# Kernel optimization log

Measured on AMD Instinct MI355X. Metric: run time of the kernel, lower is better.

The kernel has to match this reference:

```python
import jax, jax.numpy as jnp
import numpy as np

N_NODES = 100000
N_EDGES = 1600000
X_DIM, E_DIM = 4, 39


def setup_inputs() -> dict:
    key = jax.random.key(0)
    ks = jax.random.split(key, 12)
    x = jax.random.normal(ks[0], (N_NODES, X_DIM), dtype=jnp.float32)
    edge_index = jax.random.randint(ks[1], (2, N_EDGES), 0, N_NODES, dtype=jnp.int64)
    edge_attr = jax.random.normal(ks[2], (N_EDGES, E_DIM), dtype=jnp.float32)
    def lin(k, fan_in, fan_out):
        kw, kb = jax.random.split(k)
        bound = 1.0 / np.sqrt(fan_in)
        W = jax.random.uniform(kw, (fan_in, fan_out), jnp.float32, -bound, bound)
        b = jax.random.uniform(kb, (fan_out,), jnp.float32, -bound, bound)
        return W, b
    W1, b1 = lin(ks[3], 43, 64)
    W2, b2 = lin(ks[4], 64, 128)
    W3, b3 = lin(ks[5], 132, 256)
    W4, b4 = lin(ks[6], 256, 256)
    return {"x": x, "edge_index": edge_index, "edge_attr": edge_attr,
            "W1": W1, "b1": b1, "W2": W2, "b2": b2,
            "W3": W3, "b3": b3, "W4": W4, "b4": b4}


def reference(x, edge_index, edge_attr, W1, b1, W2, b2, W3, b3, W4, b4):
    row, col = edge_index[0], edge_index[1]
    n = x.shape[0]
    # gather source-node features, concat edge attrs -> edge MLP
    h = jnp.concatenate([x[col], edge_attr], axis=1)            # [E, 43]
    h = jax.nn.relu(h @ W1 + b1)                                # [E, 64]
    h = jax.nn.relu(h @ W2 + b2)                                # [E, 128]
    # scatter_mean over edges grouped by destination node `row`
    s = jax.ops.segment_sum(h, row, num_segments=n)             # [N, 128]
    cnt = jax.ops.segment_sum(jnp.ones((row.shape[0],), h.dtype), row,
                              num_segments=n)                   # [N]
    mean = s / jnp.maximum(cnt, 1.0)[:, None]                   # 0 for empty segments
    # concat node features with aggregated messages -> node MLP
    o = jnp.concatenate([x, mean], axis=1)                      # [N, 132]
    o = jax.nn.relu(o @ W3 + b3)                                # [N, 256]
    o = jax.nn.relu(o @ W4 + b4)                                # [N, 256]
    return o
```

## Files before the change

kernel.cpp:

```cpp
#include <hip/hip_runtime.h>
#include <hip/hip_bf16.h>

#define NN 100000
#define NE 1600000
#define XD 4
#define ED 39
#define K1 43
#define H1 64
#define H2 128
#define H3 256
#define NBN 16
#define NBK2 32
#define NCHUNK 98

typedef short bfrag8 __attribute__((ext_vector_type(8)));
typedef float facc4  __attribute__((ext_vector_type(4)));
typedef unsigned short u16x4 __attribute__((ext_vector_type(4)));

static __device__ __forceinline__ unsigned short f2bf(float f) {
    __hip_bfloat16 b = __float2bfloat16(f);
    union { __hip_bfloat16 b; unsigned short u; } v; v.b = b;
    return v.u;
}
static __device__ __forceinline__ float bf2f(unsigned short h) {
    union { unsigned int u; float f; } v; v.u = ((unsigned int)h) << 16;
    return v.f;
}

__global__ __launch_bounds__(256) void hist_kernel(const int* __restrict__ eidx,
                                                   int* __restrict__ cnt) {
    int e = blockIdx.x * 256 + threadIdx.x;
    if (e < NE) atomicAdd(&cnt[eidx[e]], 1);
}

__global__ __launch_bounds__(1024) void scan1_kernel(const int* __restrict__ cnt,
                                                     int* __restrict__ row_ptr,
                                                     int* __restrict__ cursor,
                                                     int* __restrict__ chunkSum) {
    __shared__ int wsum[16];
    const int t = threadIdx.x, lane = t & 63, w = t >> 6;
    const int i = blockIdx.x * 1024 + t;
    int v = (i < NN) ? cnt[i] : 0;
    int s = v;
    #pragma unroll
    for (int d = 1; d < 64; d <<= 1) {
        int u = __shfl_up(s, d, 64);
        if (lane >= d) s += u;
    }
    if (lane == 63) wsum[w] = s;
    __syncthreads();
    if (w == 0 && lane < 16) {
        int e = wsum[lane];
        #pragma unroll
        for (int d = 1; d < 16; d <<= 1) {
            int u = __shfl_up(e, d, 64);
            if (lane >= d) e += u;
        }
        wsum[lane] = e;
    }
    __syncthreads();
    int woff = (w == 0) ? 0 : wsum[w - 1];
    if (i < NN) {
        int incl = woff + s;
        row_ptr[i + 1] = incl;
        cursor[i]      = incl - v;
    }
    if (t == 0) chunkSum[blockIdx.x] = wsum[15];
}

__global__ __launch_bounds__(64) void scan2_kernel(const int* __restrict__ chunkSum,
                                                   int* __restrict__ chunkOff) {
    const int lane = threadIdx.x;
    int a = (lane < NCHUNK) ? chunkSum[lane] : 0;
    int b = (lane + 64 < NCHUNK) ? chunkSum[lane + 64] : 0;
    int sa = a;
    #pragma unroll
    for (int d = 1; d < 64; d <<= 1) {
        int u = __shfl_up(sa, d, 64);
        if (lane >= d) sa += u;
    }
    int totA = __shfl(sa, 63, 64);
    int sb = b;
    #pragma unroll
    for (int d = 1; d < 64; d <<= 1) {
        int u = __shfl_up(sb, d, 64);
        if (lane >= d) sb += u;
    }
    sb += totA;
    if (lane < NCHUNK) chunkOff[lane] = sa - a;
    if (lane + 64 < NCHUNK) chunkOff[lane + 64] = sb - b;
}

__global__ __launch_bounds__(1024) void scan3_kernel(const int* __restrict__ chunkOff,
                                                     int* __restrict__ row_ptr,
                                                     int* __restrict__ cursor) {
    const int i = blockIdx.x * 1024 + threadIdx.x;
    const int off = chunkOff[blockIdx.x];
    if (i < NN) {
        row_ptr[i + 1] += off;
        cursor[i]      += off;
    }
    if (i == 0) row_ptr[0] = 0;
}

__global__ __launch_bounds__(256) void build_kernel(const int* __restrict__ eidx,
                                                    int* __restrict__ cursor,
                                                    int* __restrict__ perm) {
    int e = blockIdx.x * 256 + threadIdx.x;
    if (e < NE) {
        int r = eidx[e];
        int pos = atomicAdd(&cursor[r], 1);
        perm[pos] = e;
    }
}

__global__ __launch_bounds__(256) void prep_kernel(
    const float* __restrict__ W1, const float* __restrict__ W2,
    const float* __restrict__ W3, const float* __restrict__ W4,
    unsigned short* __restrict__ W1h, unsigned short* __restrict__ W1l,
    unsigned short* __restrict__ W2h, unsigned short* __restrict__ W2l,
    unsigned short* __restrict__ W3h, unsigned short* __restrict__ W3l,
    unsigned short* __restrict__ W4h, unsigned short* __restrict__ W4l)
{
    int i = blockIdx.x * 256 + threadIdx.x;
    if (i >= 4096 + 8192 + 40960 + 65536) return;
    unsigned short *ph, *pl;
    int idx, col, k;
    float w;
    if (i < 4096) {
        idx = i;
        int grp = idx >> 9, lane = (idx >> 3) & 63, j = idx & 7;
        int wid = grp >> 1, ks = grp & 1;
        col = wid * 16 + (lane & 15);
        k   = ks * 32 + (lane >> 4) * 8 + j;
        w = (k < K1) ? W1[k * H1 + col] : 0.f;
        ph = W1h; pl = W1l;
    } else if (i < 12288) {
        idx = i - 4096;
        int grp = idx >> 9, lane = (idx >> 3) & 63, j = idx & 7;
        int wid = grp >> 2, nt = (grp >> 1) & 1, ks = grp & 1;
        col = wid * 32 + nt * 16 + (lane & 15);
        k   = ks * 32 + (lane >> 4) * 8 + j;
        w = W2[k * H2 + col];
        ph = W2h; pl = W2l;
    } else if (i < 53248) {
        idx = i - 12288;
        int grp = idx >> 9, lane = (idx >> 3) & 63, j = idx & 7;
        int w_ = grp / 20, rem = grp - w_ * 20;
        int ks = rem >> 2, nt = rem & 3;
        col = w_ * 64 + nt * 16 + (lane & 15);
        k   = ks * 32 + (lane >> 4) * 8 + j;
        w = (k < 132) ? W3[k * H3 + col] : 0.f;
        ph = W3h; pl = W3l;
    } else {
        idx = i - 53248;
        int grp = idx >> 9, lane = (idx >> 3) & 63, j = idx & 7;
        int w_ = grp >> 5, rem = grp & 31;
        int ks = rem >> 2, nt = rem & 3;
        col = w_ * 64 + nt * 16 + (lane & 15);
        k   = ks * 32 + (lane >> 4) * 8 + j;
        w = W4[k * H3 + col];
        ph = W4h; pl = W4l;
    }
    unsigned short h = f2bf(w);
    ph[idx] = h;
    pl[idx] = f2bf(w - bf2f(h));
}

__global__ __launch_bounds__(256, 3) void edge_agg_kernel(
    const float* __restrict__ x, const int* __restrict__ eidx,
    const float* __restrict__ ea,
    const unsigned short* __restrict__ W1h, const unsigned short* __restrict__ W1l,
    const float* __restrict__ b1,
    const unsigned short* __restrict__ W2h, const unsigned short* __restrict__ W2l,
    const float* __restrict__ b2,
    const int* __restrict__ row_ptr, const int* __restrict__ perm,
    float* __restrict__ mean)
{
    __shared__ __align__(16) unsigned short uMem[4 * 64 * 72];
    __shared__ __align__(16) int sNode[72];
    __shared__ int sPerm[2][64], sCol[2][64], sRP[NBN + 1];

    unsigned short* Ahi   = uMem;
    unsigned short* Alo   = uMem + 64 * 72;
    unsigned short* H1hi  = uMem + 2 * 64 * 72;
    unsigned short* H1lo  = uMem + 3 * 64 * 72;
    unsigned short* H2Thi = uMem;
    unsigned short* H2Tlo = uMem + 128 * 72;

    const int t    = threadIdx.x;
    const int lane = t & 63;
    const int wid  = t >> 6;
    const int cl   = lane & 15;
    const int lg   = lane >> 4;
    const int n0   = blockIdx.x * NBN;

    int p0 = -1, c0 = 0;
    if (t < 64) {
        int b0  = row_ptr[n0];
        int e0r = row_ptr[n0 + NBN];
        if (b0 + t < e0r) p0 = perm[b0 + t];
        if (p0 >= 0) c0 = eidx[NE + p0];
    }

    if (t <= NBN) sRP[t] = row_ptr[n0 + t];

    bfrag8 w1h_[2], w1l_[2], w2h_[2][2], w2l_[2][2];
    #pragma unroll
    for (int ks = 0; ks < 2; ks++) {
        const int off = ((wid * 2 + ks) * 64 + lane) * 8;
        w1h_[ks] = *(const bfrag8*)&W1h[off];
        w1l_[ks] = *(const bfrag8*)&W1l[off];
    }
    #pragma unroll
    for (int nt = 0; nt < 2; nt++)
        #pragma unroll
        for (int ks = 0; ks < 2; ks++) {
            const int off = (((wid * 2 + nt) * 2 + ks) * 64 + lane) * 8;
            w2h_[nt][ks] = *(const bfrag8*)&W2h[off];
            w2l_[nt][ks] = *(const bfrag8*)&W2l[off];
        }
    const float bias1 = b1[wid * 16 + cl];
    const float bias2[2] = { b2[wid * 32 + cl], b2[wid * 32 + 16 + cl] };

    facc4 acc_sel[2];
    #pragma unroll
    for (int nt = 0; nt < 2; nt++) {
        acc_sel[nt][0] = 0.f; acc_sel[nt][1] = 0.f;
        acc_sel[nt][2] = 0.f; acc_sel[nt][3] = 0.f;
    }

    if (t < 64) { sPerm[0][t] = p0; sCol[0][t] = c0; }
    __syncthreads();

    const int base = sRP[0], cntE = sRP[NBN] - base;

    auto loadA = [&](float (&pv)[4][4], const int* sP, const int* sC) {
        #pragma unroll
        for (int r = 0; r < 4; r++) {
            const int e  = (t >> 4) + r * 16;
            const int k0 = (t & 15) * 4;
            const int ee = sP[e];
            if (ee >= 0) {
                if (k0 == 0) {
                    float4 xv = *(const float4*)&x[(size_t)sC[e] * XD];
                    pv[r][0] = xv.x; pv[r][1] = xv.y; pv[r][2] = xv.z; pv[r][3] = xv.w;
                } else {
                    const float* er = ea + (size_t)ee * ED;
                    #pragma unroll
                    for (int q = 0; q < 4; q++) {
                        int k = k0 + q;
                        pv[r][q] = (k < K1) ? er[k - XD] : 0.f;
                    }
                }
            } else {
                pv[r][0] = pv[r][1] = pv[r][2] = pv[r][3] = 0.f;
            }
        }
    };

    if (cntE > 0) {
        float pv[4][4];
        loadA(pv, sPerm[0], sCol[0]);
        int buf = 0;

        for (int tb = 0; tb < cntE; tb += 64) {
            const int nv   = min(64, cntE - tb);
            const int nbuf = buf ^ 1;

            int pp = -1;
            if (t < 64 && tb + 64 < cntE)
                pp = (tb + 64 + t < cntE) ? perm[base + tb + 64 + t] : -1;

            #pragma unroll
            for (int r = 0; r < 4; r++) {
                const int e  = (t >> 4) + r * 16;
                const int k0 = (t & 15) * 4;
                u16x4 hv, lv;
                #pragma unroll
                for (int q = 0; q < 4; q++) {
                    unsigned short h = f2bf(pv[r][q]);
                    hv[q] = h;
                    lv[q] = f2bf(pv[r][q] - bf2f(h));
                }
                *(u16x4*)&Ahi[e * 72 + k0] = hv;
                *(u16x4*)&Alo[e * 72 + k0] = lv;
            }
            if (t < 72) {
                int nd = -1;
                if (t < nv) {
                    int idx = tb + t;
                    nd = 0;
                    #pragma unroll
                    for (int k = 1; k < 16; k++) nd += ((sRP[k] - base) <= idx);
                }
                sNode[t] = nd;
            }
            __syncthreads();

            int pc = 0;
            if (t < 64 && pp >= 0) pc = eidx[NE + pp];

            facc4 acc1[4];
            #pragma unroll
            for (int mt = 0; mt < 4; mt++) {
                acc1[mt][0] = bias1; acc1[mt][1] = bias1;
                acc1[mt][2] = bias1; acc1[mt][3] = bias1;
            }
            #pragma unroll
            for (int ks = 0; ks < 2; ks++) {
                #pragma unroll
                for (int mt = 0; mt < 4; mt++) {
                    const int ao = (mt * 16 + cl) * 72 + ks * 32 + lg * 8;
                    bfrag8 ah = *(const bfrag8*)&Ahi[ao];
                    bfrag8 al = *(const bfrag8*)&Alo[ao];
                    acc1[mt] = __builtin_amdgcn_mfma_f32_16x16x32_bf16(ah, w1h_[ks], acc1[mt], 0, 0, 0);
                    acc1[mt] = __builtin_amdgcn_mfma_f32_16x16x32_bf16(al, w1h_[ks], acc1[mt], 0, 0, 0);
                    acc1[mt] = __builtin_amdgcn_mfma_f32_16x16x32_bf16(ah, w1l_[ks], acc1[mt], 0, 0, 0);
                }
            }
            #pragma unroll
            for (int mt = 0; mt < 4; mt++)
                #pragma unroll
                for (int j = 0; j < 4; j++) {
                    float v = fmaxf(acc1[mt][j], 0.f);
                    unsigned short h = f2bf(v);
                    int m = mt * 16 + lg * 4 + j;
                    H1hi[m * 72 + wid * 16 + cl] = h;
                    H1lo[m * 72 + wid * 16 + cl] = f2bf(v - bf2f(h));
                }
            if (t < 64) { sPerm[nbuf][t] = pp; sCol[nbuf][t] = pc; }
            __syncthreads();

            if (tb + 64 < cntE) loadA(pv, sPerm[nbuf], sCol[nbuf]);

            facc4 acc2[4][2];
            #pragma unroll
            for (int mt = 0; mt < 4; mt++)
                #pragma unroll
                for (int nt = 0; nt < 2; nt++) {
                    acc2[mt][nt][0] = bias2[nt]; acc2[mt][nt][1] = bias2[nt];
                    acc2[mt][nt][2] = bias2[nt]; acc2[mt][nt][3] = bias2[nt];
                }
            #pragma unroll
            for (int ks = 0; ks < 2; ks++) {
                #pragma unroll
                for (int mt = 0; mt < 4; mt++) {
                    const int ao = (mt * 16 + cl) * 72 + ks * 32 + lg * 8;
                    bfrag8 ah = *(const bfrag8*)&H1hi[ao];
                    bfrag8 al = *(const bfrag8*)&H1lo[ao];
                    #pragma unroll
                    for (int nt = 0; nt < 2; nt++) {
                        acc2[mt][nt] = __builtin_amdgcn_mfma_f32_16x16x32_bf16(ah, w2h_[nt][ks], acc2[mt][nt], 0, 0, 0);
                        acc2[mt][nt] = __builtin_amdgcn_mfma_f32_16x16x32_bf16(al, w2h_[nt][ks], acc2[mt][nt], 0, 0, 0);
                        acc2[mt][nt] = __builtin_amdgcn_mfma_f32_16x16x32_bf16(ah, w2l_[nt][ks], acc2[mt][nt], 0, 0, 0);
                    }
                }
            }
            __syncthreads();

            #pragma unroll
            for (int mt = 0; mt < 4; mt++)
                #pragma unroll
                for (int nt = 0; nt < 2; nt++) {
                    const int c2 = wid * 32 + nt * 16 + cl;
                    u16x4 hv, lv;
                    #pragma unroll
                    for (int j = 0; j < 4; j++) {
                        float v = fmaxf(acc2[mt][nt][j], 0.f);
                        unsigned short h = f2bf(v);
                        hv[j] = h;
                        lv[j] = f2bf(v - bf2f(h));
                    }
                    const int eb = mt * 16 + lg * 4;
                    *(u16x4*)&H2Thi[c2 * 72 + eb] = hv;
                    *(u16x4*)&H2Tlo[c2 * 72 + eb] = lv;
                }
            __syncthreads();

            #pragma unroll
            for (int ks = 0; ks < 2; ks++) {
                const int4* np = (const int4*)&sNode[ks * 32 + lg * 8];
                int4 na = np[0], nb = np[1];
                bfrag8 sf;
                sf[0] = (na.x == cl) ? (short)0x3F80 : (short)0;
                sf[1] = (na.y == cl) ? (short)0x3F80 : (short)0;
                sf[2] = (na.z == cl) ? (short)0x3F80 : (short)0;
                sf[3] = (na.w == cl) ? (short)0x3F80 : (short)0;
                sf[4] = (nb.x == cl) ? (short)0x3F80 : (short)0;
                sf[5] = (nb.y == cl) ? (short)0x3F80 : (short)0;
                sf[6] = (nb.z == cl) ? (short)0x3F80 : (short)0;
                sf[7] = (nb.w == cl) ? (short)0x3F80 : (short)0;
                #pragma unroll
                for (int nt = 0; nt < 2; nt++) {
                    const int hb = (wid * 32 + nt * 16 + cl) * 72 + ks * 32 + lg * 8;
                    bfrag8 hh = *(const bfrag8*)&H2Thi[hb];
                    bfrag8 hl = *(const bfrag8*)&H2Tlo[hb];
                    acc_sel[nt] = __builtin_amdgcn_mfma_f32_16x16x32_bf16(sf, hh, acc_sel[nt], 0, 0, 0);
                    acc_sel[nt] = __builtin_amdgcn_mfma_f32_16x16x32_bf16(sf, hl, acc_sel[nt], 0, 0, 0);
                }
            }
            __syncthreads();
            buf = nbuf;
        }
    }

    #pragma unroll
    for (int nt = 0; nt < 2; nt++)
        #pragma unroll
        for (int j = 0; j < 4; j++) {
            const int n = lg * 4 + j;
            const int deg = sRP[n + 1] - sRP[n];
            const float inv = (deg > 0) ? 1.f / (float)deg : 0.f;
            mean[(size_t)(n0 + n) * H2 + wid * 32 + nt * 16 + cl] = acc_sel[nt][j] * inv;
        }
}

__global__ __launch_bounds__(256, 3) void node_kernel(
    const float* __restrict__ x,
    const float* __restrict__ mean,
    const unsigned short* __restrict__ W3h, const unsigned short* __restrict__ W3l,
    const float* __restrict__ b3,
    const unsigned short* __restrict__ W4h, const unsigned short* __restrict__ W4l,
    const float* __restrict__ b4,
    float* __restrict__ out)
{
    __shared__ __align__(16) unsigned short uM[2 * 32 * 264];
    unsigned short* Ah = uM;
    unsigned short* Al = uM + 32 * 168;
    unsigned short* Hh = uM;
    unsigned short* Hl = uM + 32 * 264;

    const int t    = threadIdx.x;
    const int lane = t & 63;
    const int w    = t >> 6;
    const int cl   = lane & 15;
    const int lg   = lane >> 4;
    const int n0   = blockIdx.x * NBK2;

    {
        const int n   = t & 31;
        const int kq0 = t >> 5;
        #pragma unroll
        for (int it = 0; it < 5; it++) {
            const int k0 = (kq0 + it * 8) * 4;
            float v[4];
            if (k0 == 0) {
                float4 xv = *(const float4*)&x[(size_t)(n0 + n) * XD];
                v[0] = xv.x; v[1] = xv.y; v[2] = xv.z; v[3] = xv.w;
            } else if (k0 <= 128) {
                float4 mv = *(const float4*)&mean[(size_t)(n0 + n) * H2 + (k0 - XD)];
                v[0] = mv.x; v[1] = mv.y; v[2] = mv.z; v[3] = mv.w;
            } else {
                v[0] = v[1] = v[2] = v[3] = 0.f;
            }
            u16x4 hv, lv;
            #pragma unroll
            for (int q = 0; q < 4; q++) {
                unsigned short h = f2bf(v[q]);
                hv[q] = h;
                lv[q] = f2bf(v[q] - bf2f(h));
            }
            *(u16x4*)&Ah[n * 168 + k0] = hv;
            *(u16x4*)&Al[n * 168 + k0] = lv;
        }
    }
    __syncthreads();

    facc4 acc[2][4];
    #pragma unroll
    for (int nt = 0; nt < 4; nt++) {
        float b = b3[w * 64 + nt * 16 + cl];
        #pragma unroll
        for (int mt = 0; mt < 2; mt++) {
            acc[mt][nt][0] = b; acc[mt][nt][1] = b;
            acc[mt][nt][2] = b; acc[mt][nt][3] = b;
        }
    }
    #pragma unroll
    for (int ks = 0; ks < 5; ks++) {
        bfrag8 ah[2], al[2];
        #pragma unroll
        for (int mt = 0; mt < 2; mt++) {
            const int ao = (mt * 16 + cl) * 168 + ks * 32 + lg * 8;
            ah[mt] = *(const bfrag8*)&Ah[ao];
            al[mt] = *(const bfrag8*)&Al[ao];
        }
        #pragma unroll
        for (int nt = 0; nt < 4; nt++) {
            const int wo = (((w * 5 + ks) * 4 + nt) * 64 + lane) * 8;
            bfrag8 bh = *(const bfrag8*)&W3h[wo];
            bfrag8 bl = *(const bfrag8*)&W3l[wo];
            #pragma unroll
            for (int mt = 0; mt < 2; mt++) {
                acc[mt][nt] = __builtin_amdgcn_mfma_f32_16x16x32_bf16(ah[mt], bh, acc[mt][nt], 0, 0, 0);
                acc[mt][nt] = __builtin_amdgcn_mfma_f32_16x16x32_bf16(al[mt], bh, acc[mt][nt], 0, 0, 0);
                acc[mt][nt] = __builtin_amdgcn_mfma_f32_16x16x32_bf16(ah[mt], bl, acc[mt][nt], 0, 0, 0);
            }
        }
    }
    __syncthreads();

    #pragma unroll
    for (int mt = 0; mt < 2; mt++)
        #pragma unroll
        for (int nt = 0; nt < 4; nt++)
            #pragma unroll
            for (int j = 0; j < 4; j++) {
                float v = fmaxf(acc[mt][nt][j], 0.f);
                const int r = mt * 16 + lg * 4 + j;
                const int c = w * 64 + nt * 16 + cl;
                unsigned short h = f2bf(v);
                Hh[r * 264 + c] = h;
                Hl[r * 264 + c] = f2bf(v - bf2f(h));
            }
    __syncthreads();

    facc4 acc2[2][4];
    #pragma unroll
    for (int nt = 0; nt < 4; nt++) {
        float b = b4[w * 64 + nt * 16 + cl];
        #pragma unroll
        for (int mt = 0; mt < 2; mt++) {
            acc2[mt][nt][0] = b; acc2[mt][nt][1] = b;
            acc2[mt][nt][2] = b; acc2[mt][nt][3] = b;
        }
    }
    #pragma unroll
    for (int ks = 0; ks < 8; ks++) {
        bfrag8 ah[2], al[2];
        #pragma unroll
        for (int mt = 0; mt < 2; mt++) {
            const int ao = (mt * 16 + cl) * 264 + ks * 32 + lg * 8;
            ah[mt] = *(const bfrag8*)&Hh[ao];
            al[mt] = *(const bfrag8*)&Hl[ao];
        }
        #pragma unroll
        for (int nt = 0; nt < 4; nt++) {
            const int wo = (((w * 8 + ks) * 4 + nt) * 64 + lane) * 8;
            bfrag8 bh = *(const bfrag8*)&W4h[wo];
            bfrag8 bl = *(const bfrag8*)&W4l[wo];
            #pragma unroll
            for (int mt = 0; mt < 2; mt++) {
                acc2[mt][nt] = __builtin_amdgcn_mfma_f32_16x16x32_bf16(ah[mt], bh, acc2[mt][nt], 0, 0, 0);
                acc2[mt][nt] = __builtin_amdgcn_mfma_f32_16x16x32_bf16(al[mt], bh, acc2[mt][nt], 0, 0, 0);
                acc2[mt][nt] = __builtin_amdgcn_mfma_f32_16x16x32_bf16(ah[mt], bl, acc2[mt][nt], 0, 0, 0);
            }
        }
    }
    #pragma unroll
    for (int mt = 0; mt < 2; mt++)
        #pragma unroll
        for (int nt = 0; nt < 4; nt++)
            #pragma unroll
            for (int j = 0; j < 4; j++)
                out[(size_t)(n0 + mt * 16 + lg * 4 + j) * H3 + w * 64 + nt * 16 + cl] =
                    fmaxf(acc2[mt][nt][j], 0.f);
}

extern "C" void kernel_launch(void* const* d_in, const int* in_sizes, int n_in,
                              void* d_out, int out_size, void* d_ws, size_t ws_size,
                              hipStream_t stream) {
    const float* x    = (const float*)d_in[0];
    const int*   eidx = (const int*)  d_in[1];
    const float* ea   = (const float*)d_in[2];
    const float* W1   = (const float*)d_in[3];
    const float* b1   = (const float*)d_in[4];
    const float* W2   = (const float*)d_in[5];
    const float* b2   = (const float*)d_in[6];
    const float* W3   = (const float*)d_in[7];
    const float* b3   = (const float*)d_in[8];
    const float* W4   = (const float*)d_in[9];
    const float* b4   = (const float*)d_in[10];
    float* out = (float*)d_out;

    char* p = (char*)d_ws;
    float* mean    = (float*)p;  p += (size_t)NN * H2 * 4;
    int*   perm    = (int*)p;    p += (size_t)NE * 4;
    int*   row_ptr = (int*)p;    p += ((size_t)NN + 8) * 4;
    int*   cursor  = (int*)p;    p += (size_t)NN * 4;
    int*   cnt     = (int*)p;    p += (size_t)NN * 4;
    int*   chunkSum = (int*)p;   p += 128 * 4;
    int*   chunkOff = (int*)p;   p += 128 * 4;

    unsigned short* wp = (unsigned short*)cursor;
    unsigned short* W1h_ = wp; wp += 64 * 64;
    unsigned short* W1l_ = wp; wp += 64 * 64;
    unsigned short* W2h_ = wp; wp += 128 * 64;
    unsigned short* W2l_ = wp; wp += 128 * 64;
    unsigned short* W3h_ = wp; wp += 256 * 160;
    unsigned short* W3l_ = wp; wp += 256 * 160;
    unsigned short* W4h_ = wp; wp += 256 * 256;
    unsigned short* W4l_ = wp; wp += 256 * 256;

    hipMemsetAsync(cnt, 0, (size_t)NN * 4, stream);

    hist_kernel <<<(NE + 255) / 256, 256, 0, stream>>>(eidx, cnt);
    scan1_kernel<<<NCHUNK, 1024, 0, stream>>>(cnt, row_ptr, cursor, chunkSum);
    scan2_kernel<<<1, 64, 0, stream>>>(chunkSum, chunkOff);
    scan3_kernel<<<NCHUNK, 1024, 0, stream>>>(chunkOff, row_ptr, cursor);
    build_kernel<<<(NE + 255) / 256, 256, 0, stream>>>(eidx, cursor, perm);
    prep_kernel <<<(4096 + 8192 + 40960 + 65536 + 255) / 256, 256, 0, stream>>>(
        W1, W2, W3, W4, W1h_, W1l_, W2h_, W2l_, W3h_, W3l_, W4h_, W4l_);
    edge_agg_kernel<<<NN / NBN, 256, 0, stream>>>(x, eidx, ea, W1h_, W1l_, b1,
                                                  W2h_, W2l_, b2, row_ptr, perm, mean);
    node_kernel<<<NN / NBK2, 256, 0, stream>>>(x, mean, W3h_, W3l_, b3,
                                               W4h_, W4l_, b4, out);
}
```

Before: 882.3 us.

## Fuse node MLP into edge aggregation kernel and drop atomics from CSR build

The node MLP (W3/W4 layers) now runs at the end of the edge aggregation kernel. The per-node mean is written as split bf16 hi/lo straight into shared memory instead of round-tripping through a global mean buffer, and the separate node kernel launch is gone. The histogram kernel also records each edge's atomic rank, so the build step computes its permutation position as row_ptr plus rank without a second atomic pass, and the cursor array is removed. In exchange, node GEMMs now use 16-row tiles, so weight fragments are fetched twice as often per node. The fused kernel may also face more register and shared-memory pressure under its occupancy bound.

```diff
diff --git a/kernel.cpp b/kernel.cpp
--- a/kernel.cpp
+++ b/kernel.cpp
@@ -10,7 +10,6 @@
 #define H2 128
 #define H3 256
 #define NBN 16
-#define NBK2 32
 #define NCHUNK 98
 
 typedef short bfrag8 __attribute__((ext_vector_type(8)));
@@ -28,14 +27,14 @@
 }
 
 __global__ __launch_bounds__(256) void hist_kernel(const int* __restrict__ eidx,
-                                                   int* __restrict__ cnt) {
+                                                   int* __restrict__ cnt,
+                                                   int* __restrict__ rank) {
     int e = blockIdx.x * 256 + threadIdx.x;
-    if (e < NE) atomicAdd(&cnt[eidx[e]], 1);
+    if (e < NE) rank[e] = atomicAdd(&cnt[eidx[e]], 1);
 }
 
 __global__ __launch_bounds__(1024) void scan1_kernel(const int* __restrict__ cnt,
                                                      int* __restrict__ row_ptr,
-                                                     int* __restrict__ cursor,
                                                      int* __restrict__ chunkSum) {
     __shared__ int wsum[16];
     const int t = threadIdx.x, lane = t & 63, w = t >> 6;
@@ -60,11 +59,7 @@
     }
     __syncthreads();
     int woff = (w == 0) ? 0 : wsum[w - 1];
-    if (i < NN) {
-        int incl = woff + s;
-        row_ptr[i + 1] = incl;
-        cursor[i]      = incl - v;
-    }
+    if (i < NN) row_ptr[i + 1] = woff + s;
     if (t == 0) chunkSum[blockIdx.x] = wsum[15];
 }
 
@@ -92,25 +87,21 @@
 }
 
 __global__ __launch_bounds__(1024) void scan3_kernel(const int* __restrict__ chunkOff,
-                                                     int* __restrict__ row_ptr,
-                                                     int* __restrict__ cursor) {
+                                                     int* __restrict__ row_ptr) {
     const int i = blockIdx.x * 1024 + threadIdx.x;
     const int off = chunkOff[blockIdx.x];
-    if (i < NN) {
-        row_ptr[i + 1] += off;
-        cursor[i]      += off;
-    }
+    if (i < NN) row_ptr[i + 1] += off;
     if (i == 0) row_ptr[0] = 0;
 }
 
 __global__ __launch_bounds__(256) void build_kernel(const int* __restrict__ eidx,
-                                                    int* __restrict__ cursor,
+                                                    const int* __restrict__ row_ptr,
+                                                    const int* __restrict__ rank,
                                                     int* __restrict__ perm) {
     int e = blockIdx.x * 256 + threadIdx.x;
     if (e < NE) {
         int r = eidx[e];
-        int pos = atomicAdd(&cursor[r], 1);
-        perm[pos] = e;
+        perm[row_ptr[r] + rank[e]] = e;
     }
 }
 
@@ -174,8 +165,12 @@
     const float* __restrict__ b1,
     const unsigned short* __restrict__ W2h, const unsigned short* __restrict__ W2l,
     const float* __restrict__ b2,
+    const unsigned short* __restrict__ W3h, const unsigned short* __restrict__ W3l,
+    const float* __restrict__ b3,
+    const unsigned short* __restrict__ W4h, const unsigned short* __restrict__ W4l,
+    const float* __restrict__ b4,
     const int* __restrict__ row_ptr, const int* __restrict__ perm,
-    float* __restrict__ mean)
+    float* __restrict__ out)
 {
     __shared__ __align__(16) unsigned short uMem[4 * 64 * 72];
     __shared__ __align__(16) int sNode[72];
@@ -187,6 +182,10 @@
     unsigned short* H1lo  = uMem + 3 * 64 * 72;
     unsigned short* H2Thi = uMem;
     unsigned short* H2Tlo = uMem + 128 * 72;
+    unsigned short* nAh   = uMem;
+    unsigned short* nAl   = uMem + 16 * 168;
+    unsigned short* Hh    = uMem + 2 * 16 * 168;
+    unsigned short* Hl    = uMem + 2 * 16 * 168 + 16 * 264;
 
     const int t    = threadIdx.x;
     const int lane = t & 63;
@@ -405,6 +404,8 @@
         }
     }
 
+    __syncthreads();
+
     #pragma unroll
     for (int nt = 0; nt < 2; nt++)
         #pragma unroll
@@ -412,150 +413,87 @@
             const int n = lg * 4 + j;
             const int deg = sRP[n + 1] - sRP[n];
             const float inv = (deg > 0) ? 1.f / (float)deg : 0.f;
-            mean[(size_t)(n0 + n) * H2 + wid * 32 + nt * 16 + cl] = acc_sel[nt][j] * inv;
-        }
-}
-
-__global__ __launch_bounds__(256, 3) void node_kernel(
-    const float* __restrict__ x,
-    const float* __restrict__ mean,
-    const unsigned short* __restrict__ W3h, const unsigned short* __restrict__ W3l,
-    const float* __restrict__ b3,
-    const unsigned short* __restrict__ W4h, const unsigned short* __restrict__ W4l,
-    const float* __restrict__ b4,
-    float* __restrict__ out)
-{
-    __shared__ __align__(16) unsigned short uM[2 * 32 * 264];
-    unsigned short* Ah = uM;
-    unsigned short* Al = uM + 32 * 168;
-    unsigned short* Hh = uM;
-    unsigned short* Hl = uM + 32 * 264;
-
-    const int t    = threadIdx.x;
-    const int lane = t & 63;
-    const int w    = t >> 6;
-    const int cl   = lane & 15;
-    const int lg   = lane >> 4;
-    const int n0   = blockIdx.x * NBK2;
-
-    {
-        const int n   = t & 31;
-        const int kq0 = t >> 5;
-        #pragma unroll
-        for (int it = 0; it < 5; it++) {
-            const int k0 = (kq0 + it * 8) * 4;
-            float v[4];
-            if (k0 == 0) {
-                float4 xv = *(const float4*)&x[(size_t)(n0 + n) * XD];
-                v[0] = xv.x; v[1] = xv.y; v[2] = xv.z; v[3] = xv.w;
-            } else if (k0 <= 128) {
-                float4 mv = *(const float4*)&mean[(size_t)(n0 + n) * H2 + (k0 - XD)];
-                v[0] = mv.x; v[1] = mv.y; v[2] = mv.z; v[3] = mv.w;
-            } else {
-                v[0] = v[1] = v[2] = v[3] = 0.f;
-            }
-            u16x4 hv, lv;
-            #pragma unroll
-            for (int q = 0; q < 4; q++) {
-                unsigned short h = f2bf(v[q]);
-                hv[q] = h;
-                lv[q] = f2bf(v[q] - bf2f(h));
-            }
-            *(u16x4*)&Ah[n * 168 + k0] = hv;
-            *(u16x4*)&Al[n * 168 + k0] = lv;
-        }
+            const float m = acc_sel[nt][j] * inv;
+            unsigned short h = f2bf(m);
+            const int k = 4 + wid * 32 + nt * 16 + cl;
+            nAh[n * 168 + k] = h;
+            nAl[n * 168 + k] = f2bf(m - bf2f(h));
+        }
+    if (t < 64) {
+        const int n = t >> 2, k = t & 3;
+        float xv = x[(size_t)(n0 + n) * XD + k];
+        unsigned short h = f2bf(xv);
+        nAh[n * 168 + k] = h;
+        nAl[n * 168 + k] = f2bf(xv - bf2f(h));
+    }
+    for (int i = t; i < 448; i += 256) {
+        int n = i / 28, k = 132 + (i - n * 28);
+        nAh[n * 168 + k] = 0;
+        nAl[n * 168 + k] = 0;
     }
     __syncthreads();
 
-    facc4 acc[2][4];
+    facc4 na_[4];
     #pragma unroll
     for (int nt = 0; nt < 4; nt++) {
-        float b = b3[w * 64 + nt * 16 + cl];
-        #pragma unroll
-        for (int mt = 0; mt < 2; mt++) {
-            acc[mt][nt][0] = b; acc[mt][nt][1] = b;
-            acc[mt][nt][2] = b; acc[mt][nt][3] = b;
-        }
+        float b = b3[wid * 64 + nt * 16 + cl];
+        na_[nt][0] = b; na_[nt][1] = b; na_[nt][2] = b; na_[nt][3] = b;
     }
     #pragma unroll
     for (int ks = 0; ks < 5; ks++) {
-        bfrag8 ah[2], al[2];
-        #pragma unroll
-        for (int mt = 0; mt < 2; mt++) {
-            const int ao = (mt * 16 + cl) * 168 + ks * 32 + lg * 8;
-            ah[mt] = *(const bfrag8*)&Ah[ao];
-            al[mt] = *(const bfrag8*)&Al[ao];
-        }
+        const int ao = cl * 168 + ks * 32 + lg * 8;
+        bfrag8 ah = *(const bfrag8*)&nAh[ao];
+        bfrag8 al = *(const bfrag8*)&nAl[ao];
         #pragma unroll
         for (int nt = 0; nt < 4; nt++) {
-            const int wo = (((w * 5 + ks) * 4 + nt) * 64 + lane) * 8;
+            const int wo = (((wid * 5 + ks) * 4 + nt) * 64 + lane) * 8;
             bfrag8 bh = *(const bfrag8*)&W3h[wo];
             bfrag8 bl = *(const bfrag8*)&W3l[wo];
-            #pragma unroll
-            for (int mt = 0; mt < 2; mt++) {
-                acc[mt][nt] = __builtin_amdgcn_mfma_f32_16x16x32_bf16(ah[mt], bh, acc[mt][nt], 0, 0, 0);
-                acc[mt][nt] = __builtin_amdgcn_mfma_f32_16x16x32_bf16(al[mt], bh, acc[mt][nt], 0, 0, 0);
-                acc[mt][nt] = __builtin_amdgcn_mfma_f32_16x16x32_bf16(ah[mt], bl, acc[mt][nt], 0, 0, 0);
-            }
-        }
-    }
+            na_[nt] = __builtin_amdgcn_mfma_f32_16x16x32_bf16(ah, bh, na_[nt], 0, 0, 0);
+            na_[nt] = __builtin_amdgcn_mfma_f32_16x16x32_bf16(al, bh, na_[nt], 0, 0, 0);
+            na_[nt] = __builtin_amdgcn_mfma_f32_16x16x32_bf16(ah, bl, na_[nt], 0, 0, 0);
+        }
+    }
+    #pragma unroll
+    for (int nt = 0; nt < 4; nt++)
+        #pragma unroll
+        for (int j = 0; j < 4; j++) {
+            float v = fmaxf(na_[nt][j], 0.f);
+            const int r = lg * 4 + j;
+            const int c = wid * 64 + nt * 16 + cl;
+            unsigned short h = f2bf(v);
+            Hh[r * 264 + c] = h;
+            Hl[r * 264 + c] = f2bf(v - bf2f(h));
+        }
     __syncthreads();
 
-    #pragma unroll
-    for (int mt = 0; mt < 2; mt++)
-        #pragma unroll
-        for (int nt = 0; nt < 4; nt++)
-            #pragma unroll
-            for (int j = 0; j < 4; j++) {
-                float v = fmaxf(acc[mt][nt][j], 0.f);
-                const int r = mt * 16 + lg * 4 + j;
-                const int c = w * 64 + nt * 16 + cl;
-                unsigned short h = f2bf(v);
-                Hh[r * 264 + c] = h;
-                Hl[r * 264 + c] = f2bf(v - bf2f(h));
-            }
-    __syncthreads();
-
-    facc4 acc2[2][4];
+    facc4 nb_[4];
     #pragma unroll
     for (int nt = 0; nt < 4; nt++) {
-        float b = b4[w * 64 + nt * 16 + cl];
-        #pragma unroll
-        for (int mt = 0; mt < 2; mt++) {
-            acc2[mt][nt][0] = b; acc2[mt][nt][1] = b;
-            acc2[mt][nt][2] = b; acc2[mt][nt][3] = b;
-        }
+        float b = b4[wid * 64 + nt * 16 + cl];
+        nb_[nt][0] = b; nb_[nt][1] = b; nb_[nt][2] = b; nb_[nt][3] = b;
     }
     #pragma unroll
     for (int ks = 0; ks < 8; ks++) {
-        bfrag8 ah[2], al[2];
-        #pragma unroll
-        for (int mt = 0; mt < 2; mt++) {
-            const int ao = (mt * 16 + cl) * 264 + ks * 32 + lg * 8;
-            ah[mt] = *(const bfrag8*)&Hh[ao];
-            al[mt] = *(const bfrag8*)&Hl[ao];
-        }
+        const int ao = cl * 264 + ks * 32 + lg * 8;
+        bfrag8 ah = *(const bfrag8*)&Hh[ao];
+        bfrag8 al = *(const bfrag8*)&Hl[ao];
         #pragma unroll
         for (int nt = 0; nt < 4; nt++) {
-            const int wo = (((w * 8 + ks) * 4 + nt) * 64 + lane) * 8;
+            const int wo = (((wid * 8 + ks) * 4 + nt) * 64 + lane) * 8;
             bfrag8 bh = *(const bfrag8*)&W4h[wo];
             bfrag8 bl = *(const bfrag8*)&W4l[wo];
-            #pragma unroll
-            for (int mt = 0; mt < 2; mt++) {
-                acc2[mt][nt] = __builtin_amdgcn_mfma_f32_16x16x32_bf16(ah[mt], bh, acc2[mt][nt], 0, 0, 0);
-                acc2[mt][nt] = __builtin_amdgcn_mfma_f32_16x16x32_bf16(al[mt], bh, acc2[mt][nt], 0, 0, 0);
-                acc2[mt][nt] = __builtin_amdgcn_mfma_f32_16x16x32_bf16(ah[mt], bl, acc2[mt][nt], 0, 0, 0);
-            }
-        }
-    }
-    #pragma unroll
-    for (int mt = 0; mt < 2; mt++)
-        #pragma unroll
-        for (int nt = 0; nt < 4; nt++)
-            #pragma unroll
-            for (int j = 0; j < 4; j++)
-                out[(size_t)(n0 + mt * 16 + lg * 4 + j) * H3 + w * 64 + nt * 16 + cl] =
-                    fmaxf(acc2[mt][nt][j], 0.f);
+            nb_[nt] = __builtin_amdgcn_mfma_f32_16x16x32_bf16(ah, bh, nb_[nt], 0, 0, 0);
+            nb_[nt] = __builtin_amdgcn_mfma_f32_16x16x32_bf16(al, bh, nb_[nt], 0, 0, 0);
+            nb_[nt] = __builtin_amdgcn_mfma_f32_16x16x32_bf16(ah, bl, nb_[nt], 0, 0, 0);
+        }
+    }
+    #pragma unroll
+    for (int nt = 0; nt < 4; nt++)
+        #pragma unroll
+        for (int j = 0; j < 4; j++)
+            out[(size_t)(n0 + lg * 4 + j) * H3 + wid * 64 + nt * 16 + cl] =
+                fmaxf(nb_[nt][j], 0.f);
 }
 
 extern "C" void kernel_launch(void* const* d_in, const int* in_sizes, int n_in,
@@ -575,15 +513,14 @@
     float* out = (float*)d_out;
 
     char* p = (char*)d_ws;
-    float* mean    = (float*)p;  p += (size_t)NN * H2 * 4;
-    int*   perm    = (int*)p;    p += (size_t)NE * 4;
-    int*   row_ptr = (int*)p;    p += ((size_t)NN + 8) * 4;
-    int*   cursor  = (int*)p;    p += (size_t)NN * 4;
-    int*   cnt     = (int*)p;    p += (size_t)NN * 4;
-    int*   chunkSum = (int*)p;   p += 128 * 4;
-    int*   chunkOff = (int*)p;   p += 128 * 4;
-
-    unsigned short* wp = (unsigned short*)cursor;
+    int* perm     = (int*)p;  p += (size_t)NE * 4;
+    int* rank     = (int*)p;  p += (size_t)NE * 4;
+    int* row_ptr  = (int*)p;  p += ((size_t)NN + 8) * 4;
+    int* cnt      = (int*)p;  p += (size_t)NN * 4;
+    int* chunkSum = (int*)p;  p += 128 * 4;
+    int* chunkOff = (int*)p;  p += 128 * 4;
+
+    unsigned short* wp = (unsigned short*)rank;
     unsigned short* W1h_ = wp; wp += 64 * 64;
     unsigned short* W1l_ = wp; wp += 64 * 64;
     unsigned short* W2h_ = wp; wp += 128 * 64;
@@ -595,15 +532,14 @@
 
     hipMemsetAsync(cnt, 0, (size_t)NN * 4, stream);
 
-    hist_kernel <<<(NE + 255) / 256, 256, 0, stream>>>(eidx, cnt);
-    scan1_kernel<<<NCHUNK, 1024, 0, stream>>>(cnt, row_ptr, cursor, chunkSum);
+    hist_kernel <<<(NE + 255) / 256, 256, 0, stream>>>(eidx, cnt, rank);
+    scan1_kernel<<<NCHUNK, 1024, 0, stream>>>(cnt, row_ptr, chunkSum);
     scan2_kernel<<<1, 64, 0, stream>>>(chunkSum, chunkOff);
-    scan3_kernel<<<NCHUNK, 1024, 0, stream>>>(chunkOff, row_ptr, cursor);
-    build_kernel<<<(NE + 255) / 256, 256, 0, stream>>>(eidx, cursor, perm);
+    scan3_kernel<<<NCHUNK, 1024, 0, stream>>>(chunkOff, row_ptr);
+    build_kernel<<<(NE + 255) / 256, 256, 0, stream>>>(eidx, row_ptr, rank, perm);
     prep_kernel <<<(4096 + 8192 + 40960 + 65536 + 255) / 256, 256, 0, stream>>>(
         W1, W2, W3, W4, W1h_, W1l_, W2h_, W2l_, W3h_, W3l_, W4h_, W4l_);
-    edge_agg_kernel<<<NN / NBN, 256, 0, stream>>>(x, eidx, ea, W1h_, W1l_, b1,
-                                                  W2h_, W2l_, b2, row_ptr, perm, mean);
-    node_kernel<<<NN / NBK2, 256, 0, stream>>>(x, mean, W3h_, W3l_, b3,
-                                               W4h_, W4l_, b4, out);
-}
+    edge_agg_kernel<<<NN / NBN, 256, 0, stream>>>(
+        x, eidx, ea, W1h_, W1l_, b1, W2h_, W2l_, b2,
+        W3h_, W3l_, b3, W4h_, W4l_, b4, row_ptr, perm, out);
+}
```

Result: faster. 778.4 us (-11.8%).
